# Performance work log

Measured on AMD Instinct MI355X. Metric: run time of the kernel, lower is better.

Reference implementation:

```python
import jax, jax.numpy as jnp
import numpy as np

D = 1024
H = 16
DH = D // H  # 64
EPS = 1e-5


def _ln(x, w, b=None):
    mu = jnp.mean(x, axis=-1, keepdims=True)
    var = jnp.var(x, axis=-1, keepdims=True)
    y = (x - mu) * jax.lax.rsqrt(var + EPS) * w
    return y + b if b is not None else y


def _rotate_half(x):
    x1, x2 = jnp.split(x, 2, axis=-1)
    return jnp.concatenate([-x2, x1], axis=-1)


def _rope(q, k):
    # q, k: [B, L, H, DH]; rotary over sequence dim (ESM-style half-split rotation)
    L = q.shape[1]
    inv_freq = 1.0 / (10000.0 ** (jnp.arange(0, DH, 2, dtype=jnp.float32) / DH))
    freqs = jnp.arange(L, dtype=jnp.float32)[:, None] * inv_freq[None, :]  # [L, DH/2]
    emb = jnp.concatenate([freqs, freqs], axis=-1)  # [L, DH]
    cos = jnp.cos(emb)[None, :, None, :]  # [1, L, 1, DH]
    sin = jnp.sin(emb)[None, :, None, :]
    q = q * cos + _rotate_half(q) * sin
    k = k * cos + _rotate_half(k) * sin
    return q, k


def setup_inputs() -> dict:
    key = jax.random.key(0)
    ks = jax.random.split(key, 8)
    B, L = 2, 2048
    x = jax.random.normal(ks[0], (B, L, D), dtype=jnp.float32)
    seq_id = jnp.sort(jax.random.randint(ks[1], (B, L), 0, 8), axis=-1)
    s = 1.0 / np.sqrt(D)
    return {
        "x": x,
        "seq_id": seq_id,
        "ln1_w": jnp.ones((D,), jnp.float32),
        "ln1_b": jnp.zeros((D,), jnp.float32),
        "w_qkv": jax.random.normal(ks[2], (3 * D, D), dtype=jnp.float32) * s,
        "q_ln_w": jnp.ones((D,), jnp.float32),
        "k_ln_w": jnp.ones((D,), jnp.float32),
        "out_w": jax.random.normal(ks[3], (D, D), dtype=jnp.float32) * s,
    }


def reference(x, seq_id, ln1_w, ln1_b, w_qkv, q_ln_w, k_ln_w, out_w):
    B, L, _ = x.shape
    h = _ln(x, ln1_w, ln1_b)
    qkv = jnp.einsum("bld,ed->ble", h, w_qkv)  # [B, L, 3D]
    q, k, v = jnp.split(qkv, 3, axis=-1)
    q = _ln(q, q_ln_w)
    k = _ln(k, k_ln_w)
    q = q.reshape(B, L, H, DH)
    k = k.reshape(B, L, H, DH)
    q, k = _rope(q, k)
    q = q.transpose(0, 2, 1, 3)  # [B, H, L, DH]
    k = k.transpose(0, 2, 1, 3)
    v = v.reshape(B, L, H, DH).transpose(0, 2, 1, 3)
    scale = 1.0 / np.sqrt(DH)
    scores = jnp.einsum("bhld,bhmd->bhlm", q, k) * scale  # [B, H, L, L]
    mask = (seq_id[:, None, :, None] == seq_id[:, None, None, :])  # [B, 1, L, L]
    scores = jnp.where(mask, scores, -jnp.inf)
    attn = jax.nn.softmax(scores, axis=-1)
    ctx = jnp.einsum("bhlm,bhmd->bhld", attn, v)  # [B, H, L, DH]
    ctx = ctx.transpose(0, 2, 1, 3).reshape(B, L, D)
    return jnp.einsum("bld,ed->ble", ctx, out_w)
```

## Files before the change

kernel.cpp:

```cpp
#include <hip/hip_runtime.h>
#include <hip/hip_bf16.h>
#include <math.h>

#define D 1024
#define H 16
#define DH 64
#define L 2048
#define B 2
#define NROW (B * L)
#define EPS 1e-5f

typedef _Float16 half8 __attribute__((ext_vector_type(8)));
typedef _Float16 half4v __attribute__((ext_vector_type(4)));
typedef float f32x4 __attribute__((ext_vector_type(4)));

__global__ __launch_bounds__(256) void ln1_fused_kernel(const float* __restrict__ x,
                                                        const float* __restrict__ lw,
                                                        const float* __restrict__ lb,
                                                        _Float16* __restrict__ h16) {
    int r = blockIdx.x;
    int t = threadIdx.x;
    const float* xr = x + (size_t)r * D;
    float4 v = *(const float4*)&xr[t * 4];
    float s = v.x + v.y + v.z + v.w;
    float sq = v.x * v.x + v.y * v.y + v.z * v.z + v.w * v.w;
    for (int off = 32; off > 0; off >>= 1) {
        s += __shfl_xor(s, off, 64);
        sq += __shfl_xor(sq, off, 64);
    }
    __shared__ float ls[4], lq[4];
    int wave = t >> 6;
    if ((t & 63) == 0) { ls[wave] = s; lq[wave] = sq; }
    __syncthreads();
    float S = ls[0] + ls[1] + ls[2] + ls[3];
    float Q = lq[0] + lq[1] + lq[2] + lq[3];
    float mu = S / (float)D;
    float rs = rsqrtf(Q / (float)D - mu * mu + EPS);
    float4 w4 = *(const float4*)&lw[t * 4];
    float4 b4 = *(const float4*)&lb[t * 4];
    half4v out = {(_Float16)((v.x - mu) * rs * w4.x + b4.x),
                  (_Float16)((v.y - mu) * rs * w4.y + b4.y),
                  (_Float16)((v.z - mu) * rs * w4.z + b4.z),
                  (_Float16)((v.w - mu) * rs * w4.w + b4.w)};
    *(half4v*)&h16[(size_t)r * D + t * 4] = out;
}

__global__ __launch_bounds__(256) void cvt_weights_kernel(const float* __restrict__ wqkv,
                                                          _Float16* __restrict__ wqkv16,
                                                          const float* __restrict__ outw,
                                                          _Float16* __restrict__ outw16) {
    int blk = blockIdx.x;
    const float* src;
    _Float16* dst;
    int base;
    if (blk < 1536) { src = wqkv; dst = wqkv16; base = blk; }
    else            { src = outw; dst = outw16; base = blk - 1536; }
    int i = (base * 256 + threadIdx.x) * 8;
    float4 a = *(const float4*)&src[i];
    float4 b = *(const float4*)&src[i + 4];
    half8 h = {(_Float16)a.x, (_Float16)a.y, (_Float16)a.z, (_Float16)a.w,
               (_Float16)b.x, (_Float16)b.y, (_Float16)b.z, (_Float16)b.w};
    *(half8*)&dst[i] = h;
}

__global__ __launch_bounds__(256) void seg_bounds_kernel(const int* __restrict__ seq_id,
                                                         int* __restrict__ lo,
                                                         int* __restrict__ hi) {
    int idx = blockIdx.x * 256 + threadIdx.x;
    if (idx >= NROW) return;
    int b = idx / L, l = idx - b * L;
    const int* row = seq_id + (size_t)b * L;
    int v = row[l];
    int a = 0, c = L;
    while (a < c) { int m = (a + c) >> 1; if (row[m] < v) a = m + 1; else c = m; }
    lo[idx] = a;
    a = 0; c = L;
    while (a < c) { int m = (a + c) >> 1; if (row[m] <= v) a = m + 1; else c = m; }
    hi[idx] = a;
}

template <typename OutT, int BM, int BN>
__global__ __launch_bounds__(256) void gemm_f16_kernel(const _Float16* __restrict__ A,
                                                       const _Float16* __restrict__ W,
                                                       OutT* __restrict__ C, int N) {
    constexpr int WM = BM / 2, WN = BN / 2;
    constexpr int MT = WM / 16, NT = WN / 16;
    __shared__ _Float16 As[BM * 32];
    __shared__ _Float16 Bs[BN * 32];
    int t = threadIdx.x;
    int w = t >> 6, lane = t & 63;
    int quad = lane >> 4, col = lane & 15;
    int m0 = blockIdx.y * BM, n0 = blockIdx.x * BN;
    int mw = (w >> 1) * WM, nw = (w & 1) * WN;
    int sw = (col >> 1) & 3;

    f32x4 acc[MT][NT] = {};

    for (int k0 = 0; k0 < 1024; k0 += 32) {
#pragma unroll
        for (int i = 0; i < BM / 64; i++) {
            int e = t + i * 256;
            int row = e >> 2, kc = (e & 3) ^ ((row >> 1) & 3);
            __builtin_amdgcn_global_load_lds(
                (const __attribute__((address_space(1))) void*)&A[(size_t)(m0 + row) * 1024 + k0 + kc * 8],
                (__attribute__((address_space(3))) void*)&As[e * 8], 16, 0, 0);
        }
#pragma unroll
        for (int i = 0; i < BN / 64; i++) {
            int e = t + i * 256;
            int row = e >> 2, kc = (e & 3) ^ ((row >> 1) & 3);
            __builtin_amdgcn_global_load_lds(
                (const __attribute__((address_space(1))) void*)&W[(size_t)(n0 + row) * 1024 + k0 + kc * 8],
                (__attribute__((address_space(3))) void*)&Bs[e * 8], 16, 0, 0);
        }
        __syncthreads();
        half8 af[MT], bf[NT];
#pragma unroll
        for (int mt = 0; mt < MT; mt++)
            af[mt] = *(const half8*)&As[(mw + mt * 16 + col) * 32 + (quad ^ sw) * 8];
#pragma unroll
        for (int nt = 0; nt < NT; nt++)
            bf[nt] = *(const half8*)&Bs[(nw + nt * 16 + col) * 32 + (quad ^ sw) * 8];
#pragma unroll
        for (int mt = 0; mt < MT; mt++)
#pragma unroll
            for (int nt = 0; nt < NT; nt++)
                acc[mt][nt] = __builtin_amdgcn_mfma_f32_16x16x32_f16(af[mt], bf[nt], acc[mt][nt], 0, 0, 0);
        __syncthreads();
    }

#pragma unroll
    for (int mt = 0; mt < MT; mt++)
#pragma unroll
        for (int nt = 0; nt < NT; nt++)
#pragma unroll
            for (int r = 0; r < 4; r++) {
                int row = m0 + mw + mt * 16 + quad * 4 + r;
                int cc = n0 + nw + nt * 16 + col;
                C[(size_t)row * N + cc] = (OutT)acc[mt][nt][r];
            }
}

__global__ __launch_bounds__(256) void qkln_rope_kernel(const _Float16* __restrict__ qkv,
                                                        const float* __restrict__ qw,
                                                        const float* __restrict__ kw,
                                                        _Float16* __restrict__ q_r,
                                                        _Float16* __restrict__ k_r) {
    int r = blockIdx.x;
    int which = blockIdx.y;
    int t = threadIdx.x;
    const _Float16* src = qkv + (size_t)r * 3072 + which * 1024;
    const float* w = which ? kw : qw;
    _Float16* dst = which ? k_r : q_r;

    float vals[4];
    float s = 0.f, sq = 0.f;
#pragma unroll
    for (int i = 0; i < 4; i++) {
        float v = (float)src[t + i * 256];
        vals[i] = v;
        s += v;
        sq += v * v;
    }
    for (int off = 32; off > 0; off >>= 1) {
        s += __shfl_xor(s, off, 64);
        sq += __shfl_xor(sq, off, 64);
    }
    __shared__ float ls[4], lq[4];
    int wave = t >> 6;
    if ((t & 63) == 0) { ls[wave] = s; lq[wave] = sq; }
    __syncthreads();
    float S = ls[0] + ls[1] + ls[2] + ls[3];
    float Q = lq[0] + lq[1] + lq[2] + lq[3];
    float mu = S / 1024.f;
    float rs = rsqrtf(Q / 1024.f - mu * mu + EPS);

    int l = r & (L - 1);
    int b = r >> 11;
#pragma unroll
    for (int i = 0; i < 4; i++) {
        int j = t + i * 256;
        float y = (vals[i] - mu) * rs * w[j];
        float p = __shfl_xor(y, 32, 64);
        int dh = j & 63, hh = j >> 6;
        int fi = dh & 31;
        float invf = expf(-(float)fi * 0.28782313662425572f);
        float angle = (float)l * invf;
        float sn, c;
        sincosf(angle, &sn, &c);
        float out = (dh < 32) ? (y * c - p * sn) : (y * c + p * sn);
        dst[((size_t)((b * H + hh) * L + l)) * 64 + dh] = (_Float16)out;
    }
}

__global__ __launch_bounds__(256) void v_extract_kernel(const _Float16* __restrict__ qkv,
                                                        _Float16* __restrict__ v_t) {
    __shared__ _Float16 T[64][72];
    int bh = blockIdx.y;
    int b = bh >> 4, h = bh & 15;
    int l0 = blockIdx.x * 64;
    int t = threadIdx.x;
#pragma unroll
    for (int i = 0; i < 2; i++) {
        int e = t + i * 256;
        int li = e >> 3, ch = e & 7;
        half8 hv = *(const half8*)&qkv[((size_t)(b * L + l0 + li)) * 3072 + 2048 + h * 64 + ch * 8];
        *(half8*)&T[li][ch * 8] = hv;
    }
    __syncthreads();
#pragma unroll
    for (int i = 0; i < 2; i++) {
        int e = t + i * 256;
        int d = e >> 3, ch = e & 7;
        half8 hv;
#pragma unroll
        for (int j = 0; j < 8; j++) hv[j] = T[ch * 8 + j][d];
        *(half8*)&v_t[((size_t)(bh * 64 + d)) * 2048 + l0 + ch * 8] = hv;
    }
}

__global__ __launch_bounds__(256) void attn_mfma_kernel(const _Float16* __restrict__ q_r,
                                                        const _Float16* __restrict__ k_r,
                                                        const _Float16* __restrict__ v_t,
                                                        const int* __restrict__ lo_arr,
                                                        const int* __restrict__ hi_arr,
                                                        _Float16* __restrict__ ctx) {
    __shared__ _Float16 Ks[64][72];
    __shared__ _Float16 VsT[64][72];
    __shared__ _Float16 Ps[4][16][72];
    int bh = blockIdx.y;
    int b = bh >> 4, h = bh & 15;
    int l0 = blockIdx.x * 64;
    int t = threadIdx.x;
    int w = t >> 6, lane = t & 63;
    int quad = lane >> 4, col = lane & 15;
    int rbase = l0 + w * 16;

    half8 qf0, qf1;
    {
        const _Float16* qp = q_r + ((size_t)(bh * L + rbase + col)) * 64 + quad * 8;
        qf0 = *(const half8*)qp;
        qf1 = *(const half8*)(qp + 32);
    }
    int myrow = rbase + quad * 4;
    int lo_r[4], hi_r[4];
#pragma unroll
    for (int r = 0; r < 4; r++) {
        lo_r[r] = lo_arr[b * L + myrow + r];
        hi_r[r] = hi_arr[b * L + myrow + r];
    }

    f32x4 o[4] = {{0.f, 0.f, 0.f, 0.f}, {0.f, 0.f, 0.f, 0.f},
                  {0.f, 0.f, 0.f, 0.f}, {0.f, 0.f, 0.f, 0.f}};
    float m_run[4], l_run[4];
#pragma unroll
    for (int r = 0; r < 4; r++) { m_run[r] = -1e30f; l_run[r] = 0.f; }

    int blo = lo_arr[b * L + l0] & ~63;
    int bhi = hi_arr[b * L + l0 + 63];

    for (int m0 = blo; m0 < bhi; m0 += 64) {
#pragma unroll
        for (int i = 0; i < 2; i++) {
            int e = t + i * 256;
            int row = e >> 3, ch = e & 7;
            *(uint4*)&Ks[row][ch * 8] =
                *(const uint4*)&k_r[((size_t)(bh * L + m0 + row)) * 64 + ch * 8];
            *(uint4*)&VsT[row][ch * 8] =
                *(const uint4*)&v_t[((size_t)(bh * 64 + row)) * 2048 + m0 + ch * 8];
        }
        __syncthreads();

        f32x4 s[4] = {{0.f, 0.f, 0.f, 0.f}, {0.f, 0.f, 0.f, 0.f},
                      {0.f, 0.f, 0.f, 0.f}, {0.f, 0.f, 0.f, 0.f}};
#pragma unroll
        for (int nt = 0; nt < 4; nt++) {
            const _Float16* kp = &Ks[nt * 16 + col][quad * 8];
            half8 kf0 = *(const half8*)kp;
            half8 kf1 = *(const half8*)(kp + 32);
            s[nt] = __builtin_amdgcn_mfma_f32_16x16x32_f16(qf0, kf0, s[nt], 0, 0, 0);
            s[nt] = __builtin_amdgcn_mfma_f32_16x16x32_f16(qf1, kf1, s[nt], 0, 0, 0);
        }

        float p[4][4];
#pragma unroll
        for (int nt = 0; nt < 4; nt++) {
            int key = m0 + nt * 16 + col;
#pragma unroll
            for (int r = 0; r < 4; r++) {
                float v = s[nt][r] * 0.125f;
                p[nt][r] = (key >= lo_r[r] && key < hi_r[r]) ? v : -INFINITY;
            }
        }

        float corr[4];
#pragma unroll
        for (int r = 0; r < 4; r++) {
            float rm = fmaxf(fmaxf(p[0][r], p[1][r]), fmaxf(p[2][r], p[3][r]));
#pragma unroll
            for (int off = 1; off < 16; off <<= 1) rm = fmaxf(rm, __shfl_xor(rm, off, 64));
            float nm = fmaxf(m_run[r], rm);
            corr[r] = __expf(m_run[r] - nm);
            m_run[r] = nm;
            float rs = 0.f;
#pragma unroll
            for (int nt = 0; nt < 4; nt++) {
                float e = __expf(p[nt][r] - nm);
                p[nt][r] = e;
                rs += e;
            }
#pragma unroll
            for (int off = 1; off < 16; off <<= 1) rs += __shfl_xor(rs, off, 64);
            l_run[r] = l_run[r] * corr[r] + rs;
        }

#pragma unroll
        for (int nt = 0; nt < 4; nt++)
#pragma unroll
            for (int r = 0; r < 4; r++) {
                o[nt][r] *= corr[r];
                Ps[w][quad * 4 + r][nt * 16 + col] = (_Float16)p[nt][r];
            }
        __syncthreads();

        half8 pf0 = *(const half8*)&Ps[w][col][quad * 8];
        half8 pf1 = *(const half8*)&Ps[w][col][32 + quad * 8];
#pragma unroll
        for (int nt = 0; nt < 4; nt++) {
            const _Float16* vp = &VsT[nt * 16 + col][quad * 8];
            half8 vf0 = *(const half8*)vp;
            half8 vf1 = *(const half8*)(vp + 32);
            o[nt] = __builtin_amdgcn_mfma_f32_16x16x32_f16(pf0, vf0, o[nt], 0, 0, 0);
            o[nt] = __builtin_amdgcn_mfma_f32_16x16x32_f16(pf1, vf1, o[nt], 0, 0, 0);
        }
        __syncthreads();
    }

#pragma unroll
    for (int nt = 0; nt < 4; nt++)
#pragma unroll
        for (int r = 0; r < 4; r++) {
            int row = myrow + r;
            ctx[((size_t)(b * L + row)) * 1024 + h * 64 + nt * 16 + col] =
                (_Float16)(o[nt][r] / l_run[r]);
        }
}

extern "C" void kernel_launch(void* const* d_in, const int* in_sizes, int n_in,
                              void* d_out, int out_size, void* d_ws, size_t ws_size,
                              hipStream_t stream) {
    const float* x      = (const float*)d_in[0];
    const int*   seq_id = (const int*)d_in[1];
    const float* ln1_w  = (const float*)d_in[2];
    const float* ln1_b  = (const float*)d_in[3];
    const float* w_qkv  = (const float*)d_in[4];
    const float* q_ln_w = (const float*)d_in[5];
    const float* k_ln_w = (const float*)d_in[6];
    const float* out_w  = (const float*)d_in[7];
    float* out = (float*)d_out;

    char* ws = (char*)d_ws;
    int*      lo     = (int*)(ws);
    int*      hi     = (int*)(ws + (64 << 10));
    _Float16* h16    = (_Float16*)(ws + (1ull << 20));
    _Float16* wqkv16 = (_Float16*)(ws + (10ull << 20));
    _Float16* outw16 = (_Float16*)(ws + (17ull << 20));
    _Float16* qkv16  = (_Float16*)(ws + (20ull << 20));
    _Float16* q_r    = (_Float16*)(ws + (45ull << 20));
    _Float16* k_r    = (_Float16*)(ws + (54ull << 20));
    _Float16* v_t    = (_Float16*)(ws + (63ull << 20));
    _Float16* ctx16  = (_Float16*)(ws + (72ull << 20));

    ln1_fused_kernel<<<dim3(NROW), dim3(256), 0, stream>>>(x, ln1_w, ln1_b, h16);
    seg_bounds_kernel<<<dim3(NROW / 256), dim3(256), 0, stream>>>(seq_id, lo, hi);
    cvt_weights_kernel<<<dim3(2048), dim3(256), 0, stream>>>(w_qkv, wqkv16, out_w, outw16);
    gemm_f16_kernel<_Float16, 128, 128><<<dim3(3072 / 128, NROW / 128), dim3(256), 0, stream>>>(
        h16, wqkv16, qkv16, 3072);
    qkln_rope_kernel<<<dim3(NROW, 2), dim3(256), 0, stream>>>(qkv16, q_ln_w, k_ln_w, q_r, k_r);
    v_extract_kernel<<<dim3(L / 64, B * H), dim3(256), 0, stream>>>(qkv16, v_t);
    attn_mfma_kernel<<<dim3(L / 64, B * H), dim3(256), 0, stream>>>(q_r, k_r, v_t, lo, hi, ctx16);
    gemm_f16_kernel<float, 64, 64><<<dim3(1024 / 64, NROW / 64), dim3(256), 0, stream>>>(
        ctx16, outw16, out, 1024);

    (void)in_sizes; (void)n_in; (void)out_size; (void)ws_size;
}
```

Baseline: 211.6 us.

## Merge prep and mid kernels, precompute rope table, deepen GEMM K tile

Three setup kernels (LN1, weight fp16 conversion, segment bounds) are merged into one prep launch, which also fills a cos/sin rope table. The Q/K norm+rope kernel and the V transpose are merged into one mid launch that reads rope factors from the table instead of calling sincos/exp per element. The GEMM now loads a K tile of 64 per iteration with an 8-way XOR swizzle, halving the number of barrier pairs at the cost of twice the shared memory. The aim is to cut launch overhead, redundant transcendental work, and synchronisation in the GEMMs.

After: 200.1 us. 1.06x faster.

```diff
diff --git a/kernel.cpp b/kernel.cpp
--- a/kernel.cpp
+++ b/kernel.cpp
@@ -14,69 +14,76 @@
 typedef _Float16 half4v __attribute__((ext_vector_type(4)));
 typedef float f32x4 __attribute__((ext_vector_type(4)));
 
-__global__ __launch_bounds__(256) void ln1_fused_kernel(const float* __restrict__ x,
-                                                        const float* __restrict__ lw,
-                                                        const float* __restrict__ lb,
-                                                        _Float16* __restrict__ h16) {
-    int r = blockIdx.x;
+__global__ __launch_bounds__(256) void prep_kernel(const float* __restrict__ x,
+                                                   const float* __restrict__ lw,
+                                                   const float* __restrict__ lb,
+                                                   _Float16* __restrict__ h16,
+                                                   const float* __restrict__ wqkv,
+                                                   _Float16* __restrict__ wqkv16,
+                                                   const float* __restrict__ outw,
+                                                   _Float16* __restrict__ outw16,
+                                                   const int* __restrict__ seq_id,
+                                                   int* __restrict__ lo,
+                                                   int* __restrict__ hi,
+                                                   float2* __restrict__ rtab) {
+    int blk = blockIdx.x;
     int t = threadIdx.x;
-    const float* xr = x + (size_t)r * D;
-    float4 v = *(const float4*)&xr[t * 4];
-    float s = v.x + v.y + v.z + v.w;
-    float sq = v.x * v.x + v.y * v.y + v.z * v.z + v.w * v.w;
-    for (int off = 32; off > 0; off >>= 1) {
-        s += __shfl_xor(s, off, 64);
-        sq += __shfl_xor(sq, off, 64);
-    }
-    __shared__ float ls[4], lq[4];
-    int wave = t >> 6;
-    if ((t & 63) == 0) { ls[wave] = s; lq[wave] = sq; }
-    __syncthreads();
-    float S = ls[0] + ls[1] + ls[2] + ls[3];
-    float Q = lq[0] + lq[1] + lq[2] + lq[3];
-    float mu = S / (float)D;
-    float rs = rsqrtf(Q / (float)D - mu * mu + EPS);
-    float4 w4 = *(const float4*)&lw[t * 4];
-    float4 b4 = *(const float4*)&lb[t * 4];
-    half4v out = {(_Float16)((v.x - mu) * rs * w4.x + b4.x),
-                  (_Float16)((v.y - mu) * rs * w4.y + b4.y),
-                  (_Float16)((v.z - mu) * rs * w4.z + b4.z),
-                  (_Float16)((v.w - mu) * rs * w4.w + b4.w)};
-    *(half4v*)&h16[(size_t)r * D + t * 4] = out;
-}
-
-__global__ __launch_bounds__(256) void cvt_weights_kernel(const float* __restrict__ wqkv,
-                                                          _Float16* __restrict__ wqkv16,
-                                                          const float* __restrict__ outw,
-                                                          _Float16* __restrict__ outw16) {
-    int blk = blockIdx.x;
-    const float* src;
-    _Float16* dst;
-    int base;
-    if (blk < 1536) { src = wqkv; dst = wqkv16; base = blk; }
-    else            { src = outw; dst = outw16; base = blk - 1536; }
-    int i = (base * 256 + threadIdx.x) * 8;
-    float4 a = *(const float4*)&src[i];
-    float4 b = *(const float4*)&src[i + 4];
-    half8 h = {(_Float16)a.x, (_Float16)a.y, (_Float16)a.z, (_Float16)a.w,
-               (_Float16)b.x, (_Float16)b.y, (_Float16)b.z, (_Float16)b.w};
-    *(half8*)&dst[i] = h;
-}
-
-__global__ __launch_bounds__(256) void seg_bounds_kernel(const int* __restrict__ seq_id,
-                                                         int* __restrict__ lo,
-                                                         int* __restrict__ hi) {
-    int idx = blockIdx.x * 256 + threadIdx.x;
-    if (idx >= NROW) return;
-    int b = idx / L, l = idx - b * L;
-    const int* row = seq_id + (size_t)b * L;
-    int v = row[l];
-    int a = 0, c = L;
-    while (a < c) { int m = (a + c) >> 1; if (row[m] < v) a = m + 1; else c = m; }
-    lo[idx] = a;
-    a = 0; c = L;
-    while (a < c) { int m = (a + c) >> 1; if (row[m] <= v) a = m + 1; else c = m; }
-    hi[idx] = a;
+    if (blk < 4096) {
+        int r = blk;
+        const float* xr = x + (size_t)r * D;
+        float4 v = *(const float4*)&xr[t * 4];
+        float s = v.x + v.y + v.z + v.w;
+        float sq = v.x * v.x + v.y * v.y + v.z * v.z + v.w * v.w;
+        for (int off = 32; off > 0; off >>= 1) {
+            s += __shfl_xor(s, off, 64);
+            sq += __shfl_xor(sq, off, 64);
+        }
+        __shared__ float ls[4], lq[4];
+        int wave = t >> 6;
+        if ((t & 63) == 0) { ls[wave] = s; lq[wave] = sq; }
+        __syncthreads();
+        float S = ls[0] + ls[1] + ls[2] + ls[3];
+        float Q = lq[0] + lq[1] + lq[2] + lq[3];
+        float mu = S / (float)D;
+        float rs = rsqrtf(Q / (float)D - mu * mu + EPS);
+        float4 w4 = *(const float4*)&lw[t * 4];
+        float4 b4 = *(const float4*)&lb[t * 4];
+        half4v o = {(_Float16)((v.x - mu) * rs * w4.x + b4.x),
+                    (_Float16)((v.y - mu) * rs * w4.y + b4.y),
+                    (_Float16)((v.z - mu) * rs * w4.z + b4.z),
+                    (_Float16)((v.w - mu) * rs * w4.w + b4.w)};
+        *(half4v*)&h16[(size_t)r * D + t * 4] = o;
+    } else if (blk < 6144) {
+        int base = blk - 4096;
+        const float* src;
+        _Float16* dst;
+        if (base < 1536) { src = wqkv; dst = wqkv16; }
+        else             { src = outw; dst = outw16; base -= 1536; }
+        int i = (base * 256 + t) * 8;
+        float4 a = *(const float4*)&src[i];
+        float4 b = *(const float4*)&src[i + 4];
+        half8 h = {(_Float16)a.x, (_Float16)a.y, (_Float16)a.z, (_Float16)a.w,
+                   (_Float16)b.x, (_Float16)b.y, (_Float16)b.z, (_Float16)b.w};
+        *(half8*)&dst[i] = h;
+    } else if (blk < 6160) {
+        int idx = (blk - 6144) * 256 + t;
+        int b = idx / L, l = idx - b * L;
+        const int* row = seq_id + (size_t)b * L;
+        int v = row[l];
+        int a = 0, c = L;
+        while (a < c) { int m = (a + c) >> 1; if (row[m] < v) a = m + 1; else c = m; }
+        lo[idx] = a;
+        a = 0; c = L;
+        while (a < c) { int m = (a + c) >> 1; if (row[m] <= v) a = m + 1; else c = m; }
+        hi[idx] = a;
+    } else {
+        int idx = (blk - 6160) * 256 + t;
+        int l = idx >> 5, fi = idx & 31;
+        float invf = expf(-(float)fi * 0.28782313662425572f);
+        float sn, cs;
+        sincosf((float)l * invf, &sn, &cs);
+        rtab[idx] = make_float2(cs, sn);
+    }
 }
 
 template <typename OutT, int BM, int BN>
@@ -85,47 +92,53 @@
                                                        OutT* __restrict__ C, int N) {
     constexpr int WM = BM / 2, WN = BN / 2;
     constexpr int MT = WM / 16, NT = WN / 16;
-    __shared__ _Float16 As[BM * 32];
-    __shared__ _Float16 Bs[BN * 32];
+    __shared__ _Float16 As[BM * 64];
+    __shared__ _Float16 Bs[BN * 64];
     int t = threadIdx.x;
     int w = t >> 6, lane = t & 63;
     int quad = lane >> 4, col = lane & 15;
     int m0 = blockIdx.y * BM, n0 = blockIdx.x * BN;
     int mw = (w >> 1) * WM, nw = (w & 1) * WN;
-    int sw = (col >> 1) & 3;
 
     f32x4 acc[MT][NT] = {};
 
-    for (int k0 = 0; k0 < 1024; k0 += 32) {
-#pragma unroll
-        for (int i = 0; i < BM / 64; i++) {
-            int e = t + i * 256;
-            int row = e >> 2, kc = (e & 3) ^ ((row >> 1) & 3);
+    for (int k0 = 0; k0 < 1024; k0 += 64) {
+#pragma unroll
+        for (int i = 0; i < BM / 32; i++) {
+            int e = t + i * 256;
+            int row = e >> 3, kc = (e & 7) ^ (row & 7);
             __builtin_amdgcn_global_load_lds(
                 (const __attribute__((address_space(1))) void*)&A[(size_t)(m0 + row) * 1024 + k0 + kc * 8],
                 (__attribute__((address_space(3))) void*)&As[e * 8], 16, 0, 0);
         }
 #pragma unroll
-        for (int i = 0; i < BN / 64; i++) {
-            int e = t + i * 256;
-            int row = e >> 2, kc = (e & 3) ^ ((row >> 1) & 3);
+        for (int i = 0; i < BN / 32; i++) {
+            int e = t + i * 256;
+            int row = e >> 3, kc = (e & 7) ^ (row & 7);
             __builtin_amdgcn_global_load_lds(
                 (const __attribute__((address_space(1))) void*)&W[(size_t)(n0 + row) * 1024 + k0 + kc * 8],
                 (__attribute__((address_space(3))) void*)&Bs[e * 8], 16, 0, 0);
         }
         __syncthreads();
-        half8 af[MT], bf[NT];
-#pragma unroll
-        for (int mt = 0; mt < MT; mt++)
-            af[mt] = *(const half8*)&As[(mw + mt * 16 + col) * 32 + (quad ^ sw) * 8];
-#pragma unroll
-        for (int nt = 0; nt < NT; nt++)
-            bf[nt] = *(const half8*)&Bs[(nw + nt * 16 + col) * 32 + (quad ^ sw) * 8];
-#pragma unroll
-        for (int mt = 0; mt < MT; mt++)
-#pragma unroll
-            for (int nt = 0; nt < NT; nt++)
-                acc[mt][nt] = __builtin_amdgcn_mfma_f32_16x16x32_f16(af[mt], bf[nt], acc[mt][nt], 0, 0, 0);
+#pragma unroll
+        for (int kk = 0; kk < 2; kk++) {
+            half8 af[MT], bf[NT];
+#pragma unroll
+            for (int mt = 0; mt < MT; mt++) {
+                int rl = mw + mt * 16 + col;
+                af[mt] = *(const half8*)&As[rl * 64 + (((kk * 4 + quad) ^ (rl & 7)) << 3)];
+            }
+#pragma unroll
+            for (int nt = 0; nt < NT; nt++) {
+                int rl = nw + nt * 16 + col;
+                bf[nt] = *(const half8*)&Bs[rl * 64 + (((kk * 4 + quad) ^ (rl & 7)) << 3)];
+            }
+#pragma unroll
+            for (int mt = 0; mt < MT; mt++)
+#pragma unroll
+                for (int nt = 0; nt < NT; nt++)
+                    acc[mt][nt] = __builtin_amdgcn_mfma_f32_16x16x32_f16(af[mt], bf[nt], acc[mt][nt], 0, 0, 0);
+        }
         __syncthreads();
     }
 
@@ -141,81 +154,79 @@
             }
 }
 
-__global__ __launch_bounds__(256) void qkln_rope_kernel(const _Float16* __restrict__ qkv,
-                                                        const float* __restrict__ qw,
-                                                        const float* __restrict__ kw,
-                                                        _Float16* __restrict__ q_r,
-                                                        _Float16* __restrict__ k_r) {
-    int r = blockIdx.x;
-    int which = blockIdx.y;
+__global__ __launch_bounds__(256) void mid_kernel(const _Float16* __restrict__ qkv,
+                                                  const float* __restrict__ qw,
+                                                  const float* __restrict__ kw,
+                                                  const float2* __restrict__ rtab,
+                                                  _Float16* __restrict__ q_r,
+                                                  _Float16* __restrict__ k_r,
+                                                  _Float16* __restrict__ v_t) {
+    __shared__ float ls[4], lq[4];
+    __shared__ _Float16 T[64][72];
+    int blk = blockIdx.x;
     int t = threadIdx.x;
-    const _Float16* src = qkv + (size_t)r * 3072 + which * 1024;
-    const float* w = which ? kw : qw;
-    _Float16* dst = which ? k_r : q_r;
-
-    float vals[4];
-    float s = 0.f, sq = 0.f;
-#pragma unroll
-    for (int i = 0; i < 4; i++) {
-        float v = (float)src[t + i * 256];
-        vals[i] = v;
-        s += v;
-        sq += v * v;
-    }
-    for (int off = 32; off > 0; off >>= 1) {
-        s += __shfl_xor(s, off, 64);
-        sq += __shfl_xor(sq, off, 64);
-    }
-    __shared__ float ls[4], lq[4];
-    int wave = t >> 6;
-    if ((t & 63) == 0) { ls[wave] = s; lq[wave] = sq; }
-    __syncthreads();
-    float S = ls[0] + ls[1] + ls[2] + ls[3];
-    float Q = lq[0] + lq[1] + lq[2] + lq[3];
-    float mu = S / 1024.f;
-    float rs = rsqrtf(Q / 1024.f - mu * mu + EPS);
-
-    int l = r & (L - 1);
-    int b = r >> 11;
-#pragma unroll
-    for (int i = 0; i < 4; i++) {
-        int j = t + i * 256;
-        float y = (vals[i] - mu) * rs * w[j];
-        float p = __shfl_xor(y, 32, 64);
-        int dh = j & 63, hh = j >> 6;
-        int fi = dh & 31;
-        float invf = expf(-(float)fi * 0.28782313662425572f);
-        float angle = (float)l * invf;
-        float sn, c;
-        sincosf(angle, &sn, &c);
-        float out = (dh < 32) ? (y * c - p * sn) : (y * c + p * sn);
-        dst[((size_t)((b * H + hh) * L + l)) * 64 + dh] = (_Float16)out;
-    }
-}
-
-__global__ __launch_bounds__(256) void v_extract_kernel(const _Float16* __restrict__ qkv,
-                                                        _Float16* __restrict__ v_t) {
-    __shared__ _Float16 T[64][72];
-    int bh = blockIdx.y;
-    int b = bh >> 4, h = bh & 15;
-    int l0 = blockIdx.x * 64;
-    int t = threadIdx.x;
-#pragma unroll
-    for (int i = 0; i < 2; i++) {
-        int e = t + i * 256;
-        int li = e >> 3, ch = e & 7;
-        half8 hv = *(const half8*)&qkv[((size_t)(b * L + l0 + li)) * 3072 + 2048 + h * 64 + ch * 8];
-        *(half8*)&T[li][ch * 8] = hv;
-    }
-    __syncthreads();
-#pragma unroll
-    for (int i = 0; i < 2; i++) {
-        int e = t + i * 256;
-        int d = e >> 3, ch = e & 7;
-        half8 hv;
-#pragma unroll
-        for (int j = 0; j < 8; j++) hv[j] = T[ch * 8 + j][d];
-        *(half8*)&v_t[((size_t)(bh * 64 + d)) * 2048 + l0 + ch * 8] = hv;
+    if (blk < 8192) {
+        int r = blk >> 1;
+        int which = blk & 1;
+        const _Float16* src = qkv + (size_t)r * 3072 + which * 1024;
+        const float* w = which ? kw : qw;
+        _Float16* dst = which ? k_r : q_r;
+
+        float vals[4];
+        float s = 0.f, sq = 0.f;
+#pragma unroll
+        for (int i = 0; i < 4; i++) {
+            float v = (float)src[t + i * 256];
+            vals[i] = v;
+            s += v;
+            sq += v * v;
+        }
+        for (int off = 32; off > 0; off >>= 1) {
+            s += __shfl_xor(s, off, 64);
+            sq += __shfl_xor(sq, off, 64);
+        }
+        int wave = t >> 6;
+        if ((t & 63) == 0) { ls[wave] = s; lq[wave] = sq; }
+        __syncthreads();
+        float S = ls[0] + ls[1] + ls[2] + ls[3];
+        float Q = lq[0] + lq[1] + lq[2] + lq[3];
+        float mu = S / 1024.f;
+        float rs = rsqrtf(Q / 1024.f - mu * mu + EPS);
+
+        int l = r & (L - 1);
+        int b = r >> 11;
+#pragma unroll
+        for (int i = 0; i < 4; i++) {
+            int j = t + i * 256;
+            float y = (vals[i] - mu) * rs * w[j];
+            float p = __shfl_xor(y, 32, 64);
+            int dh = j & 63, hh = j >> 6;
+            float2 cs = rtab[l * 32 + (dh & 31)];
+            float out = (dh < 32) ? (y * cs.x - p * cs.y) : (y * cs.x + p * cs.y);
+            dst[((size_t)((b * H + hh) * L + l)) * 64 + dh] = (_Float16)out;
+        }
+    } else {
+        int vb = blk - 8192;
+        int bh = vb >> 5;
+        int b = bh >> 4, h = bh & 15;
+        int l0 = (vb & 31) * 64;
+#pragma unroll
+        for (int i = 0; i < 2; i++) {
+            int e = t + i * 256;
+            int li = e >> 3, ch = e & 7;
+            half8 hv = *(const half8*)&qkv[((size_t)(b * L + l0 + li)) * 3072 + 2048 + h * 64 + ch * 8];
+            *(half8*)&T[li][ch * 8] = hv;
+        }
+        __syncthreads();
+#pragma unroll
+        for (int i = 0; i < 2; i++) {
+            int e = t + i * 256;
+            int d = e >> 3, ch = e & 7;
+            half8 hv;
+#pragma unroll
+            for (int j = 0; j < 8; j++) hv[j] = T[ch * 8 + j][d];
+            *(half8*)&v_t[((size_t)(bh * 64 + d)) * 2048 + l0 + ch * 8] = hv;
+        }
     }
 }
 
@@ -362,6 +373,7 @@
     char* ws = (char*)d_ws;
     int*      lo     = (int*)(ws);
     int*      hi     = (int*)(ws + (64 << 10));
+    float2*   rtab   = (float2*)(ws + (128 << 10));
     _Float16* h16    = (_Float16*)(ws + (1ull << 20));
     _Float16* wqkv16 = (_Float16*)(ws + (10ull << 20));
     _Float16* outw16 = (_Float16*)(ws + (17ull << 20));
@@ -371,13 +383,11 @@
     _Float16* v_t    = (_Float16*)(ws + (63ull << 20));
     _Float16* ctx16  = (_Float16*)(ws + (72ull << 20));
 
-    ln1_fused_kernel<<<dim3(NROW), dim3(256), 0, stream>>>(x, ln1_w, ln1_b, h16);
-    seg_bounds_kernel<<<dim3(NROW / 256), dim3(256), 0, stream>>>(seq_id, lo, hi);
-    cvt_weights_kernel<<<dim3(2048), dim3(256), 0, stream>>>(w_qkv, wqkv16, out_w, outw16);
+    prep_kernel<<<dim3(6416), dim3(256), 0, stream>>>(
+        x, ln1_w, ln1_b, h16, w_qkv, wqkv16, out_w, outw16, seq_id, lo, hi, rtab);
     gemm_f16_kernel<_Float16, 128, 128><<<dim3(3072 / 128, NROW / 128), dim3(256), 0, stream>>>(
         h16, wqkv16, qkv16, 3072);
-    qkln_rope_kernel<<<dim3(NROW, 2), dim3(256), 0, stream>>>(qkv16, q_ln_w, k_ln_w, q_r, k_r);
-    v_extract_kernel<<<dim3(L / 64, B * H), dim3(256), 0, stream>>>(qkv16, v_t);
+    mid_kernel<<<dim3(9216), dim3(256), 0, stream>>>(qkv16, q_ln_w, k_ln_w, rtab, q_r, k_r, v_t);
     attn_mfma_kernel<<<dim3(L / 64, B * H), dim3(256), 0, stream>>>(q_r, k_r, v_t, lo, hi, ctx16);
     gemm_f16_kernel<float, 64, 64><<<dim3(1024 / 64, NROW / 64), dim3(256), 0, stream>>>(
         ctx16, outw16, out, 1024);
```
